# Optimization experiments

Measured on AMD Instinct MI355X. Metric: run time of the kernel, lower is better.

The kernel has to match this reference:

```python
import jax, jax.numpy as jnp
import numpy as np

BETA = 0.5
THR = 1.0
BN_EPS = 1e-5

@jax.custom_vjp
def spike(x):
    # heaviside fire: spk = 1[x > 0]
    return (x > 0).astype(x.dtype)

def _spike_fwd(x):
    return spike(x), x

def _spike_bwd(x, g):
    # snnTorch surrogate.atan(), alpha=2: grad = (alpha/2) / (1 + (pi/2*alpha*x)^2) = 1/(1+(pi*x)^2)
    return (g / (1.0 + (jnp.pi * x) ** 2),)

spike.defvjp(_spike_fwd, _spike_bwd)

def setup_inputs() -> dict:
    key = jax.random.key(0)
    ks = jax.random.split(key, 6)
    B, T, D, O = 512, 128, 512, 10
    data = jax.random.normal(ks[0], (B, T, D), dtype=jnp.float32)
    # deterministic Dropout(0.5) mask in {0, 2} (scaled by 1/keep_prob), time-major
    u = jax.random.uniform(ks[1], (T, B, D), dtype=jnp.float32)
    drop_mask = (u > 0.5).astype(jnp.float32) * 2.0
    W1 = jax.random.normal(ks[2], (D, D), dtype=jnp.float32) / np.sqrt(D)
    b1 = jax.random.normal(ks[3], (D,), dtype=jnp.float32) * 0.01
    gamma = jnp.ones((D,), dtype=jnp.float32)
    bn_beta = jnp.zeros((D,), dtype=jnp.float32)
    W2 = jax.random.normal(ks[4], (O, D), dtype=jnp.float32) / np.sqrt(D)
    b2 = jax.random.normal(ks[5], (O,), dtype=jnp.float32) * 0.01
    return {"data": data, "drop_mask": drop_mask, "W1": W1, "b1": b1,
            "gamma": gamma, "bn_beta": bn_beta, "W2": W2, "b2": b2}

def reference(data, drop_mask, W1, b1, gamma, bn_beta, W2, b2):
    B, T, D = data.shape
    O = W2.shape[0]
    xs = jnp.transpose(data, (1, 0, 2))  # [T, B, D] time-major

    def batchnorm(x):  # training-mode BatchNorm1d over batch dim
        mean = jnp.mean(x, axis=0)
        var = jnp.mean((x - mean) ** 2, axis=0)
        return gamma * (x - mean) * jax.lax.rsqrt(var + BN_EPS) + bn_beta

    def step(carry, inp):
        mem1, spk1, mem2, spk2 = carry
        xt, mt = inp
        cur1 = batchnorm((mt * xt) @ W1.T + b1)          # dropout -> linear -> BN
        mem1 = BETA * mem1 + cur1 - spk1 * THR           # Leaky, subtract reset
        spk1 = spike(mem1 - THR)
        cur2 = spk1 @ W2.T + b2
        mem2 = BETA * mem2 + cur2 - spk2 * THR
        spk2 = spike(mem2 - THR)
        return (mem1, spk1, mem2, spk2), spk2

    init = (jnp.zeros((B, D), data.dtype), jnp.zeros((B, D), data.dtype),
            jnp.zeros((B, O), data.dtype), jnp.zeros((B, O), data.dtype))
    _, spk_rec = jax.lax.scan(step, init, (xs, drop_mask))
    return spk_rec  # [T, B, out_size] == torch.stack(spk_rec)
```

## Files before the change

kernel.cpp:

```cpp
#include <hip/hip_runtime.h>
#include <math.h>

#define B_ 512
#define T_ 128
#define D_ 512
#define O_ 10

typedef unsigned int uint32;
typedef unsigned long long uint64;
typedef short bf16x8 __attribute__((ext_vector_type(8)));
typedef float f32x4 __attribute__((ext_vector_type(4)));

__device__ __forceinline__ uint32 bf16rne(float f) {
    uint32 u = __float_as_uint(f);
    return (u + 0x7FFFu + ((u >> 16) & 1u)) >> 16;
}
__device__ __forceinline__ float bf16f(uint32 h) { return __uint_as_float(h << 16); }

__device__ __forceinline__ uint32 pkbf16(float lo, float hi) {
    return bf16rne(lo) | (bf16rne(hi) << 16);
}

__device__ __forceinline__ void gload16_lds(const void* g, void* l) {
    __builtin_amdgcn_global_load_lds(
        (const __attribute__((address_space(1))) unsigned int*)g,
        (__attribute__((address_space(3))) unsigned int*)l, 16, 0, 0);
}

__global__ __launch_bounds__(256)
void presplitW_kernel(const float* __restrict__ W1, unsigned short* __restrict__ Wsp)
{
    const int idx = blockIdx.x * 256 + threadIdx.x;
    const float4 v = *(const float4*)(W1 + (size_t)idx * 4);
    float vv[4] = {v.x, v.y, v.z, v.w};
    uint32 c0[4], c1[4], c2[4];
#pragma unroll
    for (int i = 0; i < 4; ++i) {
        c0[i] = bf16rne(vv[i]);
        float r = vv[i] - bf16f(c0[i]);
        c1[i] = bf16rne(r);
        float r2 = r - bf16f(c1[i]);
        c2[i] = bf16rne(r2);
    }
    const size_t base = (size_t)idx * 4;
    uint2 w;
    w.x = c0[0] | (c0[1] << 16); w.y = c0[2] | (c0[3] << 16);
    *(uint2*)(Wsp + base) = w;
    w.x = c1[0] | (c1[1] << 16); w.y = c1[2] | (c1[3] << 16);
    *(uint2*)(Wsp + 262144 + base) = w;
    w.x = c2[0] | (c2[1] << 16); w.y = c2[2] | (c2[3] << 16);
    *(uint2*)(Wsp + 524288 + base) = w;
}

#define SPW 32
#define SPL (128*SPW)

__global__ __launch_bounds__(256)
void gemm1_kernel(const float* __restrict__ data, const float* __restrict__ drop,
                  const unsigned short* __restrict__ Wsp, const float* __restrict__ b1,
                  float* __restrict__ hbuf, double* __restrict__ pSum,
                  double* __restrict__ pSq, int t0, int Tc)
{
    __shared__ __align__(16) unsigned short As3[3 * SPL];
    __shared__ __align__(16) unsigned short Ws3[2][3 * SPL];

    const int tid = threadIdx.x;
    const int bid = blockIdx.x;
    const int xcd = bid & 7;
    const int rest = bid >> 3;
    const int yy = rest & 3;
    const int g = (rest >> 2) * 8 + xcd;

    const int R = g * 128;
    const int tc = R >> 9;
    const int b_base = R & 511;
    const int t = t0 + tc;
    const int d0 = yy * 128;

    const int w = tid >> 6;
    const int lane = tid & 63;
    const int wm = w & 1, wn = w >> 1;
    const int q = lane >> 4, r16 = lane & 15;

    f32x4 acc[4][4];
#pragma unroll
    for (int i = 0; i < 4; ++i)
#pragma unroll
        for (int j = 0; j < 4; ++j) acc[i][j] = (f32x4){0.f, 0.f, 0.f, 0.f};

    int dstA[2];
    const float* dsrc[2];
    const float* msrc[2];
#pragma unroll
    for (int i = 0; i < 2; ++i) {
        const int p = tid + i * 256;
        const int m = p >> 2;
        const int qg = p & 3;
        dstA[i] = m * SPW + (qg ^ ((m >> 1) & 3)) * 8;
        dsrc[i] = data + ((size_t)(b_base + m) * T_ + t) * D_ + qg * 8;
        msrc[i] = drop + ((size_t)t * B_ + b_base + m) * D_ + qg * 8;
    }

#define STAGE_W(K0, BUF)                                                        \
    {                                                                           \
        _Pragma("unroll")                                                       \
        for (int i_ = 0; i_ < 6; ++i_) {                                        \
            const int p_ = tid + i_ * 256;                                      \
            const int s_ = p_ >> 9;                                             \
            const int rem_ = p_ & 511;                                          \
            const int n_ = rem_ >> 2;                                           \
            const int qs_ = rem_ & 3;                                           \
            const int qg_ = qs_ ^ ((n_ >> 1) & 3);                              \
            gload16_lds(Wsp + (size_t)s_ * 262144 + (size_t)(d0 + n_) * 512     \
                            + (K0) + qg_ * 8,                                   \
                        &Ws3[BUF][(size_t)p_ * 8]);                             \
        }                                                                       \
    }

    STAGE_W(0, 0);
    float4 dR[2][2], mR[2][2];
#pragma unroll
    for (int i = 0; i < 2; ++i) {
        dR[i][0] = *(const float4*)(dsrc[i]);
        dR[i][1] = *(const float4*)(dsrc[i] + 4);
        mR[i][0] = *(const float4*)(msrc[i]);
        mR[i][1] = *(const float4*)(msrc[i] + 4);
    }

    int cur = 0;
    for (int ks = 0; ks < 16; ++ks) {
        const int k0 = ks * 32;
        if (ks < 15) STAGE_W(k0 + 32, cur ^ 1);

#pragma unroll
        for (int i = 0; i < 2; ++i) {
            float vv[8] = {dR[i][0].x*mR[i][0].x, dR[i][0].y*mR[i][0].y,
                           dR[i][0].z*mR[i][0].z, dR[i][0].w*mR[i][0].w,
                           dR[i][1].x*mR[i][1].x, dR[i][1].y*mR[i][1].y,
                           dR[i][1].z*mR[i][1].z, dR[i][1].w*mR[i][1].w};
            uint32 q0[4], q1[4], q2[4];
#pragma unroll
            for (int pr = 0; pr < 4; ++pr) {
                const float a = vv[2*pr], b = vv[2*pr+1];
                q0[pr] = pkbf16(a, b);
                const float ra = a - __uint_as_float(q0[pr] << 16);
                const float rb = b - __uint_as_float(q0[pr] & 0xFFFF0000u);
                q1[pr] = pkbf16(ra, rb);
                const float sa = ra - __uint_as_float(q1[pr] << 16);
                const float sb = rb - __uint_as_float(q1[pr] & 0xFFFF0000u);
                q2[pr] = pkbf16(sa, sb);
            }
            uint4 pk;
            pk.x = q0[0]; pk.y = q0[1]; pk.z = q0[2]; pk.w = q0[3];
            *(uint4*)(&As3[dstA[i]]) = pk;
            pk.x = q1[0]; pk.y = q1[1]; pk.z = q1[2]; pk.w = q1[3];
            *(uint4*)(&As3[SPL + dstA[i]]) = pk;
            pk.x = q2[0]; pk.y = q2[1]; pk.z = q2[2]; pk.w = q2[3];
            *(uint4*)(&As3[2*SPL + dstA[i]]) = pk;
        }

        if (ks < 15) {
            const int kn = k0 + 32;
#pragma unroll
            for (int i = 0; i < 2; ++i) {
                dR[i][0] = *(const float4*)(dsrc[i] + kn);
                dR[i][1] = *(const float4*)(dsrc[i] + kn + 4);
                mR[i][0] = *(const float4*)(msrc[i] + kn);
                mR[i][1] = *(const float4*)(msrc[i] + kn + 4);
            }
        }

        __builtin_amdgcn_sched_barrier(0);
        asm volatile("s_waitcnt lgkmcnt(0)");
        __builtin_amdgcn_s_barrier();
        __builtin_amdgcn_sched_barrier(0);

        const int qa = q ^ ((r16 >> 1) & 3);
        bf16x8 af[4][3], bfr[4][3];
#pragma unroll
        for (int mt = 0; mt < 4; ++mt)
#pragma unroll
            for (int s = 0; s < 3; ++s)
                af[mt][s] = *(const bf16x8*)(&As3[s*SPL + (wm*64 + mt*16 + r16)*SPW + qa*8]);
#pragma unroll
        for (int nt = 0; nt < 4; ++nt)
#pragma unroll
            for (int s = 0; s < 3; ++s)
                bfr[nt][s] = *(const bf16x8*)(&Ws3[cur][s*SPL + (wn*64 + nt*16 + r16)*SPW + qa*8]);

        __builtin_amdgcn_s_setprio(1);
#define PRODUCT(SA, SB)                                                          \
        {                                                                        \
            _Pragma("unroll")                                                    \
            for (int mt = 0; mt < 4; ++mt) {                                     \
                _Pragma("unroll")                                                \
                for (int nt = 0; nt < 4; ++nt)                                   \
                    acc[mt][nt] = __builtin_amdgcn_mfma_f32_16x16x32_bf16(       \
                        af[mt][SA], bfr[nt][SB], acc[mt][nt], 0, 0, 0);          \
            }                                                                    \
        }
        PRODUCT(0, 0)
        PRODUCT(0, 1)
        PRODUCT(1, 0)
        PRODUCT(1, 1)
        PRODUCT(0, 2)
        PRODUCT(2, 0)
#undef PRODUCT
        __builtin_amdgcn_s_setprio(0);

        __builtin_amdgcn_sched_barrier(0);
        __builtin_amdgcn_s_barrier();
        __builtin_amdgcn_sched_barrier(0);
        cur ^= 1;
    }
#undef STAGE_W

    float b1c[4];
#pragma unroll
    for (int nt = 0; nt < 4; ++nt) b1c[nt] = b1[d0 + wn*64 + nt*16 + r16];

    double sd[4], sq[4];
#pragma unroll
    for (int nt = 0; nt < 4; ++nt) { sd[nt] = 0.0; sq[nt] = 0.0; }

#pragma unroll
    for (int mt = 0; mt < 4; ++mt)
#pragma unroll
        for (int r = 0; r < 4; ++r) {
            const int row = R + wm*64 + mt*16 + q*4 + r;
            float* op = hbuf + (size_t)row * D_ + d0 + wn*64 + r16;
#pragma unroll
            for (int nt = 0; nt < 4; ++nt) {
                const float hf = acc[mt][nt][r] + b1c[nt];
                op[nt*16] = hf;
                const double dh = (double)hf;
                sd[nt] += dh;
                sq[nt] = fma(dh, dh, sq[nt]);
            }
        }
#pragma unroll
    for (int nt = 0; nt < 4; ++nt) {
        sd[nt] += __shfl_xor(sd[nt], 16); sd[nt] += __shfl_xor(sd[nt], 32);
        sq[nt] += __shfl_xor(sq[nt], 16); sq[nt] += __shfl_xor(sq[nt], 32);
    }
    double* dsh = (double*)&As3[0];
    __syncthreads();
    if (q == 0) {
#pragma unroll
        for (int nt = 0; nt < 4; ++nt) {
            dsh[(w*64 + nt*16 + r16)*2 + 0] = sd[nt];
            dsh[(w*64 + nt*16 + r16)*2 + 1] = sq[nt];
        }
    }
    __syncthreads();
    if (tid < 128) {
        const int col = tid;
        const int gg = col >> 6, c = col & 63;
        const double S = dsh[((2*gg)*64 + c)*2 + 0] + dsh[((2*gg+1)*64 + c)*2 + 0];
        const double Q = dsh[((2*gg)*64 + c)*2 + 1] + dsh[((2*gg+1)*64 + c)*2 + 1];
        const int bt = b_base >> 7;
        pSum[((size_t)(bt*Tc + tc))*D_ + d0 + col] = S;
        pSq [((size_t)(bt*Tc + tc))*D_ + d0 + col] = Q;
    }
}

__global__ __launch_bounds__(256)
void finalize_kernel(const double* __restrict__ pSum, const double* __restrict__ pSq,
                     const float* __restrict__ gamma, const float* __restrict__ bn_beta,
                     float* __restrict__ scaleArr, float* __restrict__ shiftArr, int Tc)
{
    const int tc = blockIdx.x;
    const int d = blockIdx.y * 256 + threadIdx.x;
    double S = 0.0, Q = 0.0;
#pragma unroll
    for (int bt = 0; bt < 4; ++bt) {
        S += pSum[((size_t)(bt * Tc + tc)) * D_ + d];
        Q += pSq [((size_t)(bt * Tc + tc)) * D_ + d];
    }
    const double mean = S / (double)B_;
    const double var  = Q / (double)B_ - mean * mean;
    const double rs   = 1.0 / sqrt(var + 1e-5);
    const double gm   = (double)gamma[d] * rs;
    scaleArr[tc * D_ + d] = (float)gm;
    shiftArr[tc * D_ + d] = (float)((double)bn_beta[d] - gm * mean);
}

__global__ __launch_bounds__(256)
void scanA_kernel(const float* __restrict__ hbuf, const float* __restrict__ scaleArr,
                  const float* __restrict__ shiftArr, uint64* __restrict__ spkM,
                  float* __restrict__ sMem1, float* __restrict__ sSpk1, int t0, int Tc)
{
    const int e = blockIdx.x * 256 + threadIdx.x;
    const int d = e & 511;
    const int lane = threadIdx.x & 63;
    const int mword = (e >> 6);

    float m1, s1;
    if (t0 == 0) { m1 = 0.f; s1 = 0.f; }
    else { m1 = sMem1[e]; s1 = sSpk1[e]; }

    float hv[4], sc[4], sf[4];
#pragma unroll
    for (int j = 0; j < 4; ++j) {
        const int tcj = (j < Tc) ? j : (Tc - 1);
        hv[j] = hbuf[(size_t)tcj * (B_ * D_) + e];
        sc[j] = scaleArr[tcj * D_ + d];
        sf[j] = shiftArr[tcj * D_ + d];
    }

    for (int tc = 0; tc < Tc; tc += 4) {
        float hvN[4], scN[4], sfN[4];
#pragma unroll
        for (int j = 0; j < 4; ++j) {
            int tn = tc + 4 + j; tn = (tn < Tc) ? tn : (Tc - 1);
            hvN[j] = hbuf[(size_t)tn * (B_ * D_) + e];
            scN[j] = scaleArr[tn * D_ + d];
            sfN[j] = shiftArr[tn * D_ + d];
        }
#pragma unroll
        for (int j = 0; j < 4; ++j) {
            if (tc + j < Tc) {
                const float cur1 = fmaf(sc[j], hv[j], sf[j]);
                m1 = fmaf(0.5f, m1, cur1) - s1;
                s1 = ((m1 - 1.0f) > 0.f) ? 1.f : 0.f;
                const uint64 mask = __ballot(s1 == 1.f);
                if (lane == 0)
                    spkM[(size_t)(tc + j) * (B_ * 8) + mword] = mask;
            }
        }
#pragma unroll
        for (int j = 0; j < 4; ++j) { hv[j] = hvN[j]; sc[j] = scN[j]; sf[j] = sfN[j]; }
    }

    sMem1[e] = m1;
    sSpk1[e] = s1;
}

__global__ __launch_bounds__(256)
void gemm2_kernel(const uint64* __restrict__ spkM, const float* __restrict__ W2,
                  const float* __restrict__ b2, float* __restrict__ cur2)
{
    const int g = blockIdx.x * 256 + threadIdx.x;
    const int row = g >> 3;
    const int i = g & 7;
    const unsigned char* sp = (const unsigned char*)spkM;

    float P[8][O_];
#pragma unroll
    for (int c = 0; c < 8; ++c) {
        const uint32 byte = sp[(size_t)row * 64 + c * 8 + i];
        float f[8];
#pragma unroll
        for (int j = 0; j < 8; ++j)
            f[j] = (byte & (1u << j)) ? 1.0f : 0.0f;
#pragma unroll
        for (int o = 0; o < O_; ++o) {
            const float* wp = W2 + o * D_ + (i + 8 * c) * 8;
            const float4 wa = *(const float4*)(wp);
            const float4 wb = *(const float4*)(wp + 4);
            float v = f[0] * wa.x;
            v = fmaf(f[1], wa.y, v); v = fmaf(f[2], wa.z, v); v = fmaf(f[3], wa.w, v);
            v = fmaf(f[4], wb.x, v); v = fmaf(f[5], wb.y, v); v = fmaf(f[6], wb.z, v);
            v = fmaf(f[7], wb.w, v);
            P[c][o] = v;
        }
    }

    float p[O_];
#pragma unroll
    for (int o = 0; o < O_; ++o) {
        const float a1 = P[0][o] + P[4][o];
        const float a2 = P[2][o] + P[6][o];
        const float a3 = P[1][o] + P[5][o];
        const float a4 = P[3][o] + P[7][o];
        p[o] = (a1 + a2) + (a3 + a4);
    }
#pragma unroll
    for (int o = 0; o < O_; ++o) {
        p[o] += __shfl_xor(p[o], 4);
        p[o] += __shfl_xor(p[o], 2);
        p[o] += __shfl_xor(p[o], 1);
    }

    float out0 = 0.f, out1 = 0.f;
#pragma unroll
    for (int o = 0; o < 8; ++o)
        if (i == o) out0 = p[o] + b2[o];
    if (i == 0) out1 = p[8] + b2[8];
    if (i == 1) out1 = p[9] + b2[9];
    cur2[(size_t)row * O_ + i] = out0;
    if (i < 2)
        cur2[(size_t)row * O_ + 8 + i] = out1;
}

__global__ __launch_bounds__(256)
void scanB_kernel(const float* __restrict__ cur2, float* __restrict__ out,
                  float* __restrict__ sMem2, float* __restrict__ sSpk2, int t0, int Tc)
{
    const int idx = blockIdx.x * 256 + threadIdx.x;
    float mem2, spk2;
    if (t0 == 0) { mem2 = 0.f; spk2 = 0.f; }
    else { mem2 = sMem2[idx]; spk2 = sSpk2[idx]; }

    float v[4], vn[4];
#pragma unroll
    for (int j = 0; j < 4; ++j) v[j] = cur2[(size_t)j * (B_ * O_) + idx];

    for (int tg = 0; tg < Tc; tg += 4) {
        if (tg + 4 < Tc) {
#pragma unroll
            for (int j = 0; j < 4; ++j)
                vn[j] = cur2[(size_t)(tg + 4 + j) * (B_ * O_) + idx];
        }
#pragma unroll
        for (int j = 0; j < 4; ++j) {
            mem2 = fmaf(0.5f, mem2, v[j]) - spk2;
            spk2 = ((mem2 - 1.0f) > 0.f) ? 1.f : 0.f;
            out[(size_t)(t0 + tg + j) * (B_ * O_) + idx] = spk2;
        }
#pragma unroll
        for (int j = 0; j < 4; ++j) v[j] = vn[j];
    }
    sMem2[idx] = mem2;
    sSpk2[idx] = spk2;
}

extern "C" void kernel_launch(void* const* d_in, const int* in_sizes, int n_in,
                              void* d_out, int out_size, void* d_ws, size_t ws_size,
                              hipStream_t stream) {
    const float* data    = (const float*)d_in[0];
    const float* drop    = (const float*)d_in[1];
    const float* W1      = (const float*)d_in[2];
    const float* b1      = (const float*)d_in[3];
    const float* gamma   = (const float*)d_in[4];
    const float* bn_beta = (const float*)d_in[5];
    const float* W2      = (const float*)d_in[6];
    const float* b2      = (const float*)d_in[7];
    float* out = (float*)d_out;

    const size_t fixedBytes = 1572864 + 2*1048576 + 2*20480;
    const size_t perT = 1048576 + 32768 + 20480 + 4096 + 32768;
    int Tc = T_;
    while (Tc > 2 && fixedBytes + (size_t)Tc * perT > ws_size) Tc >>= 1;

    char* p = (char*)d_ws;
    double* pSum    = (double*)p; p += (size_t)4 * Tc * D_ * 8;
    double* pSq     = (double*)p; p += (size_t)4 * Tc * D_ * 8;
    float* hbuf     = (float*)p; p += (size_t)Tc * B_ * D_ * 4;
    float* scaleArr = (float*)p; p += (size_t)Tc * D_ * 4;
    float* shiftArr = (float*)p; p += (size_t)Tc * D_ * 4;
    float* sMem1    = (float*)p; p += (size_t)B_ * D_ * 4;
    float* sSpk1    = (float*)p; p += (size_t)B_ * D_ * 4;
    float* sMem2    = (float*)p; p += (size_t)B_ * O_ * 4;
    float* sSpk2    = (float*)p; p += (size_t)B_ * O_ * 4;
    float* cur2     = (float*)p; p += (size_t)Tc * B_ * O_ * 4;
    unsigned short* Wsp = (unsigned short*)p; p += (size_t)3 * D_ * D_ * 2;
    uint64* spkM    = (uint64*)p; p += (size_t)Tc * B_ * 8 * 8;

    presplitW_kernel<<<256, 256, 0, stream>>>(W1, Wsp);

    for (int t0 = 0; t0 < T_; t0 += Tc) {
        gemm1_kernel<<<Tc * 16, 256, 0, stream>>>(data, drop, Wsp, b1, hbuf,
                                                  pSum, pSq, t0, Tc);
        finalize_kernel<<<dim3(Tc, D_ / 256), 256, 0, stream>>>(
            pSum, pSq, gamma, bn_beta, scaleArr, shiftArr, Tc);
        scanA_kernel<<<(B_ * D_) / 256, 256, 0, stream>>>(hbuf, scaleArr, shiftArr, spkM,
                                                          sMem1, sSpk1, t0, Tc);
        gemm2_kernel<<<Tc * 16, 256, 0, stream>>>(spkM, W2, b2, cur2);
        scanB_kernel<<<20, 256, 0, stream>>>(cur2, out, sMem2, sSpk2, t0, Tc);
    }
}
```

Before: 506.6 us.

## Fuse BN finalize into scan and gemm2 with output scan, use atomic stats

The per-batch-tile partial sums for the batch-norm statistics are now accumulated with double-precision atomics into a single per-time buffer. The separate finalize kernel is removed, and scanA recomputes the BN scale and shift inline in double precision for every element. gemm2 and scanB are merged into one kernel per batch row that keeps cur2 in LDS, removing the cur2 global buffer and two launches. In exchange, scanA does redundant double-precision divides and sqrt per element, the fused scan runs serially on only 10 threads per block, and double atomics add contention.

```diff
diff --git a/kernel.cpp b/kernel.cpp
--- a/kernel.cpp
+++ b/kernel.cpp
@@ -28,9 +28,11 @@
 }
 
 __global__ __launch_bounds__(256)
-void presplitW_kernel(const float* __restrict__ W1, unsigned short* __restrict__ Wsp)
+void presplitW_kernel(const float* __restrict__ W1, unsigned short* __restrict__ Wsp,
+                      double* __restrict__ pSum, double* __restrict__ pSq, int nAcc)
 {
     const int idx = blockIdx.x * 256 + threadIdx.x;
+    if (idx < nAcc) { pSum[idx] = 0.0; pSq[idx] = 0.0; }
     const float4 v = *(const float4*)(W1 + (size_t)idx * 4);
     float vv[4] = {v.x, v.y, v.z, v.w};
     uint32 c0[4], c1[4], c2[4];
@@ -258,36 +260,15 @@
         const int gg = col >> 6, c = col & 63;
         const double S = dsh[((2*gg)*64 + c)*2 + 0] + dsh[((2*gg+1)*64 + c)*2 + 0];
         const double Q = dsh[((2*gg)*64 + c)*2 + 1] + dsh[((2*gg+1)*64 + c)*2 + 1];
-        const int bt = b_base >> 7;
-        pSum[((size_t)(bt*Tc + tc))*D_ + d0 + col] = S;
-        pSq [((size_t)(bt*Tc + tc))*D_ + d0 + col] = Q;
+        atomicAdd(&pSum[tc * D_ + d0 + col], S);
+        atomicAdd(&pSq [tc * D_ + d0 + col], Q);
     }
 }
 
 __global__ __launch_bounds__(256)
-void finalize_kernel(const double* __restrict__ pSum, const double* __restrict__ pSq,
-                     const float* __restrict__ gamma, const float* __restrict__ bn_beta,
-                     float* __restrict__ scaleArr, float* __restrict__ shiftArr, int Tc)
-{
-    const int tc = blockIdx.x;
-    const int d = blockIdx.y * 256 + threadIdx.x;
-    double S = 0.0, Q = 0.0;
-#pragma unroll
-    for (int bt = 0; bt < 4; ++bt) {
-        S += pSum[((size_t)(bt * Tc + tc)) * D_ + d];
-        Q += pSq [((size_t)(bt * Tc + tc)) * D_ + d];
-    }
-    const double mean = S / (double)B_;
-    const double var  = Q / (double)B_ - mean * mean;
-    const double rs   = 1.0 / sqrt(var + 1e-5);
-    const double gm   = (double)gamma[d] * rs;
-    scaleArr[tc * D_ + d] = (float)gm;
-    shiftArr[tc * D_ + d] = (float)((double)bn_beta[d] - gm * mean);
-}
-
-__global__ __launch_bounds__(256)
-void scanA_kernel(const float* __restrict__ hbuf, const float* __restrict__ scaleArr,
-                  const float* __restrict__ shiftArr, uint64* __restrict__ spkM,
+void scanA_kernel(const float* __restrict__ hbuf, const double* __restrict__ pSum,
+                  const double* __restrict__ pSq, const float* __restrict__ gamma,
+                  const float* __restrict__ bn_beta, uint64* __restrict__ spkM,
                   float* __restrict__ sMem1, float* __restrict__ sSpk1, int t0, int Tc)
 {
     const int e = blockIdx.x * 256 + threadIdx.x;
@@ -295,32 +276,41 @@
     const int lane = threadIdx.x & 63;
     const int mword = (e >> 6);
 
+    const double gmA = (double)gamma[d];
+    const double btA = (double)bn_beta[d];
+
     float m1, s1;
     if (t0 == 0) { m1 = 0.f; s1 = 0.f; }
     else { m1 = sMem1[e]; s1 = sSpk1[e]; }
 
-    float hv[4], sc[4], sf[4];
+    float hv[4]; double Sv[4], Qv[4];
 #pragma unroll
     for (int j = 0; j < 4; ++j) {
         const int tcj = (j < Tc) ? j : (Tc - 1);
         hv[j] = hbuf[(size_t)tcj * (B_ * D_) + e];
-        sc[j] = scaleArr[tcj * D_ + d];
-        sf[j] = shiftArr[tcj * D_ + d];
+        Sv[j] = pSum[tcj * D_ + d];
+        Qv[j] = pSq [tcj * D_ + d];
     }
 
     for (int tc = 0; tc < Tc; tc += 4) {
-        float hvN[4], scN[4], sfN[4];
+        float hvN[4]; double SvN[4], QvN[4];
 #pragma unroll
         for (int j = 0; j < 4; ++j) {
             int tn = tc + 4 + j; tn = (tn < Tc) ? tn : (Tc - 1);
             hvN[j] = hbuf[(size_t)tn * (B_ * D_) + e];
-            scN[j] = scaleArr[tn * D_ + d];
-            sfN[j] = shiftArr[tn * D_ + d];
+            SvN[j] = pSum[tn * D_ + d];
+            QvN[j] = pSq [tn * D_ + d];
         }
 #pragma unroll
         for (int j = 0; j < 4; ++j) {
             if (tc + j < Tc) {
-                const float cur1 = fmaf(sc[j], hv[j], sf[j]);
+                const double mean = Sv[j] / (double)B_;
+                const double var  = Qv[j] / (double)B_ - mean * mean;
+                const double rs   = 1.0 / sqrt(var + 1e-5);
+                const double gm   = gmA * rs;
+                const float sc = (float)gm;
+                const float sf = (float)(btA - gm * mean);
+                const float cur1 = fmaf(sc, hv[j], sf);
                 m1 = fmaf(0.5f, m1, cur1) - s1;
                 s1 = ((m1 - 1.0f) > 0.f) ? 1.f : 0.f;
                 const uint64 mask = __ballot(s1 == 1.f);
@@ -329,7 +319,7 @@
             }
         }
 #pragma unroll
-        for (int j = 0; j < 4; ++j) { hv[j] = hvN[j]; sc[j] = scN[j]; sf[j] = sfN[j]; }
+        for (int j = 0; j < 4; ++j) { hv[j] = hvN[j]; Sv[j] = SvN[j]; Qv[j] = QvN[j]; }
     }
 
     sMem1[e] = m1;
@@ -337,92 +327,68 @@
 }
 
 __global__ __launch_bounds__(256)
-void gemm2_kernel(const uint64* __restrict__ spkM, const float* __restrict__ W2,
-                  const float* __restrict__ b2, float* __restrict__ cur2)
+void gemm2scanB_kernel(const uint64* __restrict__ spkM, const float* __restrict__ W2,
+                       const float* __restrict__ b2, float* __restrict__ out,
+                       float* __restrict__ sMem2, float* __restrict__ sSpk2,
+                       double* __restrict__ pSum, double* __restrict__ pSq,
+                       int t0, int Tc)
 {
-    const int g = blockIdx.x * 256 + threadIdx.x;
-    const int row = g >> 3;
-    const int i = g & 7;
-    const unsigned char* sp = (const unsigned char*)spkM;
-
-    float P[8][O_];
-#pragma unroll
-    for (int c = 0; c < 8; ++c) {
-        const uint32 byte = sp[(size_t)row * 64 + c * 8 + i];
-        float f[8];
-#pragma unroll
-        for (int j = 0; j < 8; ++j)
-            f[j] = (byte & (1u << j)) ? 1.0f : 0.0f;
-#pragma unroll
-        for (int o = 0; o < O_; ++o) {
-            const float* wp = W2 + o * D_ + (i + 8 * c) * 8;
-            const float4 wa = *(const float4*)(wp);
-            const float4 wb = *(const float4*)(wp + 4);
-            float v = f[0] * wa.x;
-            v = fmaf(f[1], wa.y, v); v = fmaf(f[2], wa.z, v); v = fmaf(f[3], wa.w, v);
-            v = fmaf(f[4], wb.x, v); v = fmaf(f[5], wb.y, v); v = fmaf(f[6], wb.z, v);
-            v = fmaf(f[7], wb.w, v);
-            P[c][o] = v;
-        }
-    }
-
-    float p[O_];
-#pragma unroll
-    for (int o = 0; o < O_; ++o) {
-        const float a1 = P[0][o] + P[4][o];
-        const float a2 = P[2][o] + P[6][o];
-        const float a3 = P[1][o] + P[5][o];
-        const float a4 = P[3][o] + P[7][o];
-        p[o] = (a1 + a2) + (a3 + a4);
-    }
-#pragma unroll
-    for (int o = 0; o < O_; ++o) {
-        p[o] += __shfl_xor(p[o], 4);
-        p[o] += __shfl_xor(p[o], 2);
-        p[o] += __shfl_xor(p[o], 1);
-    }
-
-    float out0 = 0.f, out1 = 0.f;
-#pragma unroll
-    for (int o = 0; o < 8; ++o)
-        if (i == o) out0 = p[o] + b2[o];
-    if (i == 0) out1 = p[8] + b2[8];
-    if (i == 1) out1 = p[9] + b2[9];
-    cur2[(size_t)row * O_ + i] = out0;
-    if (i < 2)
-        cur2[(size_t)row * O_ + 8 + i] = out1;
-}
-
-__global__ __launch_bounds__(256)
-void scanB_kernel(const float* __restrict__ cur2, float* __restrict__ out,
-                  float* __restrict__ sMem2, float* __restrict__ sSpk2, int t0, int Tc)
-{
-    const int idx = blockIdx.x * 256 + threadIdx.x;
-    float mem2, spk2;
-    if (t0 == 0) { mem2 = 0.f; spk2 = 0.f; }
-    else { mem2 = sMem2[idx]; spk2 = sSpk2[idx]; }
-
-    float v[4], vn[4];
-#pragma unroll
-    for (int j = 0; j < 4; ++j) v[j] = cur2[(size_t)j * (B_ * O_) + idx];
-
-    for (int tg = 0; tg < Tc; tg += 4) {
-        if (tg + 4 < Tc) {
-#pragma unroll
-            for (int j = 0; j < 4; ++j)
-                vn[j] = cur2[(size_t)(tg + 4 + j) * (B_ * O_) + idx];
-        }
-#pragma unroll
-        for (int j = 0; j < 4; ++j) {
-            mem2 = fmaf(0.5f, mem2, v[j]) - spk2;
+    __shared__ float c2s[128][O_];
+    const int b = blockIdx.x;
+    const int tid = threadIdx.x;
+    const int t = tid >> 1;
+    const int oh = (tid & 1) * 5;
+
+    if (t < Tc) {
+        const int row = t * B_ + b;
+        uint64 mk[8];
+#pragma unroll
+        for (int c = 0; c < 8; ++c) mk[c] = spkM[(size_t)row * 8 + c];
+#pragma unroll
+        for (int oo = 0; oo < 5; ++oo) {
+            const int o = oh + oo;
+            float T[8];
+#pragma unroll
+            for (int i = 0; i < 8; ++i) {
+                float P[8];
+#pragma unroll
+                for (int c = 0; c < 8; ++c) {
+                    const uint32 byte = (uint32)(mk[c] >> (i * 8)) & 0xFFu;
+                    float f[8];
+#pragma unroll
+                    for (int j = 0; j < 8; ++j)
+                        f[j] = (byte & (1u << j)) ? 1.0f : 0.0f;
+                    const float* wp = W2 + o * D_ + (i + 8 * c) * 8;
+                    const float4 wa = *(const float4*)(wp);
+                    const float4 wb = *(const float4*)(wp + 4);
+                    float v = f[0] * wa.x;
+                    v = fmaf(f[1], wa.y, v); v = fmaf(f[2], wa.z, v); v = fmaf(f[3], wa.w, v);
+                    v = fmaf(f[4], wb.x, v); v = fmaf(f[5], wb.y, v); v = fmaf(f[6], wb.z, v);
+                    v = fmaf(f[7], wb.w, v);
+                    P[c] = v;
+                }
+                T[i] = ((P[0] + P[4]) + (P[2] + P[6])) + ((P[1] + P[5]) + (P[3] + P[7]));
+            }
+            const float p = ((T[0] + T[4]) + (T[2] + T[6])) + ((T[1] + T[5]) + (T[3] + T[7]));
+            c2s[t][o] = p + b2[o];
+        }
+    }
+    __syncthreads();
+    if (tid < O_) {
+        const int o = tid;
+        float mem2, spk2;
+        if (t0 == 0) { mem2 = 0.f; spk2 = 0.f; }
+        else { mem2 = sMem2[b * O_ + o]; spk2 = sSpk2[b * O_ + o]; }
+        for (int tt = 0; tt < Tc; ++tt) {
+            mem2 = fmaf(0.5f, mem2, c2s[tt][o]) - spk2;
             spk2 = ((mem2 - 1.0f) > 0.f) ? 1.f : 0.f;
-            out[(size_t)(t0 + tg + j) * (B_ * O_) + idx] = spk2;
-        }
-#pragma unroll
-        for (int j = 0; j < 4; ++j) v[j] = vn[j];
-    }
-    sMem2[idx] = mem2;
-    sSpk2[idx] = spk2;
+            out[(size_t)(t0 + tt) * (B_ * O_) + b * O_ + o] = spk2;
+        }
+        sMem2[b * O_ + o] = mem2;
+        sSpk2[b * O_ + o] = spk2;
+    }
+    const int idx = b * 256 + tid;
+    if (idx < Tc * D_) { pSum[idx] = 0.0; pSq[idx] = 0.0; }
 }
 
 extern "C" void kernel_launch(void* const* d_in, const int* in_sizes, int n_in,
@@ -439,34 +405,30 @@
     float* out = (float*)d_out;
 
     const size_t fixedBytes = 1572864 + 2*1048576 + 2*20480;
-    const size_t perT = 1048576 + 32768 + 20480 + 4096 + 32768;
+    const size_t perT = 1048576 + 32768 + 8192;
     int Tc = T_;
     while (Tc > 2 && fixedBytes + (size_t)Tc * perT > ws_size) Tc >>= 1;
 
     char* p = (char*)d_ws;
-    double* pSum    = (double*)p; p += (size_t)4 * Tc * D_ * 8;
-    double* pSq     = (double*)p; p += (size_t)4 * Tc * D_ * 8;
+    double* pSum    = (double*)p; p += (size_t)Tc * D_ * 8;
+    double* pSq     = (double*)p; p += (size_t)Tc * D_ * 8;
     float* hbuf     = (float*)p; p += (size_t)Tc * B_ * D_ * 4;
-    float* scaleArr = (float*)p; p += (size_t)Tc * D_ * 4;
-    float* shiftArr = (float*)p; p += (size_t)Tc * D_ * 4;
     float* sMem1    = (float*)p; p += (size_t)B_ * D_ * 4;
     float* sSpk1    = (float*)p; p += (size_t)B_ * D_ * 4;
     float* sMem2    = (float*)p; p += (size_t)B_ * O_ * 4;
     float* sSpk2    = (float*)p; p += (size_t)B_ * O_ * 4;
-    float* cur2     = (float*)p; p += (size_t)Tc * B_ * O_ * 4;
     unsigned short* Wsp = (unsigned short*)p; p += (size_t)3 * D_ * D_ * 2;
     uint64* spkM    = (uint64*)p; p += (size_t)Tc * B_ * 8 * 8;
 
-    presplitW_kernel<<<256, 256, 0, stream>>>(W1, Wsp);
+    presplitW_kernel<<<256, 256, 0, stream>>>(W1, Wsp, pSum, pSq, Tc * D_);
 
     for (int t0 = 0; t0 < T_; t0 += Tc) {
         gemm1_kernel<<<Tc * 16, 256, 0, stream>>>(data, drop, Wsp, b1, hbuf,
                                                   pSum, pSq, t0, Tc);
-        finalize_kernel<<<dim3(Tc, D_ / 256), 256, 0, stream>>>(
-            pSum, pSq, gamma, bn_beta, scaleArr, shiftArr, Tc);
-        scanA_kernel<<<(B_ * D_) / 256, 256, 0, stream>>>(hbuf, scaleArr, shiftArr, spkM,
-                                                          sMem1, sSpk1, t0, Tc);
-        gemm2_kernel<<<Tc * 16, 256, 0, stream>>>(spkM, W2, b2, cur2);
-        scanB_kernel<<<20, 256, 0, stream>>>(cur2, out, sMem2, sSpk2, t0, Tc);
-    }
-}
+        scanA_kernel<<<(B_ * D_) / 256, 256, 0, stream>>>(hbuf, pSum, pSq, gamma,
+                                                          bn_beta, spkM, sMem1, sSpk1,
+                                                          t0, Tc);
+        gemm2scanB_kernel<<<B_, 256, 0, stream>>>(spkM, W2, b2, out, sMem2, sSpk2,
+                                                  pSum, pSq, t0, Tc);
+    }
+}
```

Result: slower. 572.6 us (+13.0%).

## Build GEMM A fragments directly in registers instead of staging through LDS

Applied to the files above, without the earlier changes.

The masked input tile is now loaded by each wave straight from global memory in MFMA fragment order. It is split into three bf16 parts in registers rather than written to a shared As3 buffer and read back. This removes the As3 LDS buffer, its writes and reads, and the barrier that sat between producing and consuming A. The W barrier's reuse of that buffer's space for the reduction scratch moves to Ws3. In exchange, the two waves that share the same rows both load and convert those rows, which doubles global A traffic and the split arithmetic per block. Removing that barrier also risks a race on the asynchronously loaded W buffer if no other synchronisation remains in the loop.

```diff
diff --git a/kernel.cpp b/kernel.cpp
--- a/kernel.cpp
+++ b/kernel.cpp
@@ -61,7 +61,6 @@
                   float* __restrict__ hbuf, double* __restrict__ pSum,
                   double* __restrict__ pSq, int t0, int Tc)
 {
-    __shared__ __align__(16) unsigned short As3[3 * SPL];
     __shared__ __align__(16) unsigned short Ws3[2][3 * SPL];
 
     const int tid = threadIdx.x;
@@ -88,18 +87,11 @@
 #pragma unroll
         for (int j = 0; j < 4; ++j) acc[i][j] = (f32x4){0.f, 0.f, 0.f, 0.f};
 
-    int dstA[2];
-    const float* dsrc[2];
-    const float* msrc[2];
-#pragma unroll
-    for (int i = 0; i < 2; ++i) {
-        const int p = tid + i * 256;
-        const int m = p >> 2;
-        const int qg = p & 3;
-        dstA[i] = m * SPW + (qg ^ ((m >> 1) & 3)) * 8;
-        dsrc[i] = data + ((size_t)(b_base + m) * T_ + t) * D_ + qg * 8;
-        msrc[i] = drop + ((size_t)t * B_ + b_base + m) * D_ + qg * 8;
-    }
+    const int row0 = b_base + wm * 64 + r16;
+    const float* dsrc0 = data + ((size_t)row0 * T_ + t) * D_ + q * 8;
+    const float* msrc0 = drop + ((size_t)t * B_ + row0) * D_ + q * 8;
+    const size_t dStride = (size_t)16 * T_ * D_;
+    const size_t mStride = (size_t)16 * D_;
 
 #define STAGE_W(K0, BUF)                                                        \
     {                                                                           \
@@ -118,13 +110,13 @@
     }
 
     STAGE_W(0, 0);
-    float4 dR[2][2], mR[2][2];
-#pragma unroll
-    for (int i = 0; i < 2; ++i) {
-        dR[i][0] = *(const float4*)(dsrc[i]);
-        dR[i][1] = *(const float4*)(dsrc[i] + 4);
-        mR[i][0] = *(const float4*)(msrc[i]);
-        mR[i][1] = *(const float4*)(msrc[i] + 4);
+    float4 dR[4][2], mR[4][2];
+#pragma unroll
+    for (int mt = 0; mt < 4; ++mt) {
+        dR[mt][0] = *(const float4*)(dsrc0 + (size_t)mt * dStride);
+        dR[mt][1] = *(const float4*)(dsrc0 + (size_t)mt * dStride + 4);
+        mR[mt][0] = *(const float4*)(msrc0 + (size_t)mt * mStride);
+        mR[mt][1] = *(const float4*)(msrc0 + (size_t)mt * mStride + 4);
     }
 
     int cur = 0;
@@ -132,12 +124,13 @@
         const int k0 = ks * 32;
         if (ks < 15) STAGE_W(k0 + 32, cur ^ 1);
 
-#pragma unroll
-        for (int i = 0; i < 2; ++i) {
-            float vv[8] = {dR[i][0].x*mR[i][0].x, dR[i][0].y*mR[i][0].y,
-                           dR[i][0].z*mR[i][0].z, dR[i][0].w*mR[i][0].w,
-                           dR[i][1].x*mR[i][1].x, dR[i][1].y*mR[i][1].y,
-                           dR[i][1].z*mR[i][1].z, dR[i][1].w*mR[i][1].w};
+        bf16x8 af[4][3];
+#pragma unroll
+        for (int mt = 0; mt < 4; ++mt) {
+            float vv[8] = {dR[mt][0].x*mR[mt][0].x, dR[mt][0].y*mR[mt][0].y,
+                           dR[mt][0].z*mR[mt][0].z, dR[mt][0].w*mR[mt][0].w,
+                           dR[mt][1].x*mR[mt][1].x, dR[mt][1].y*mR[mt][1].y,
+                           dR[mt][1].z*mR[mt][1].z, dR[mt][1].w*mR[mt][1].w};
             uint32 q0[4], q1[4], q2[4];
 #pragma unroll
             for (int pr = 0; pr < 4; ++pr) {
@@ -150,43 +143,32 @@
                 const float sb = rb - __uint_as_float(q1[pr] & 0xFFFF0000u);
                 q2[pr] = pkbf16(sa, sb);
             }
-            uint4 pk;
-            pk.x = q0[0]; pk.y = q0[1]; pk.z = q0[2]; pk.w = q0[3];
-            *(uint4*)(&As3[dstA[i]]) = pk;
-            pk.x = q1[0]; pk.y = q1[1]; pk.z = q1[2]; pk.w = q1[3];
-            *(uint4*)(&As3[SPL + dstA[i]]) = pk;
-            pk.x = q2[0]; pk.y = q2[1]; pk.z = q2[2]; pk.w = q2[3];
-            *(uint4*)(&As3[2*SPL + dstA[i]]) = pk;
-        }
+            union { uint32 u[4]; bf16x8 v; } c0, c1, c2;
+#pragma unroll
+            for (int pr = 0; pr < 4; ++pr) {
+                c0.u[pr] = q0[pr]; c1.u[pr] = q1[pr]; c2.u[pr] = q2[pr];
+            }
+            af[mt][0] = c0.v; af[mt][1] = c1.v; af[mt][2] = c2.v;
+        }
+
+        const int qa = q ^ ((r16 >> 1) & 3);
+        bf16x8 bfr[4][3];
+#pragma unroll
+        for (int nt = 0; nt < 4; ++nt)
+#pragma unroll
+            for (int s = 0; s < 3; ++s)
+                bfr[nt][s] = *(const bf16x8*)(&Ws3[cur][s*SPL + (wn*64 + nt*16 + r16)*SPW + qa*8]);
 
         if (ks < 15) {
             const int kn = k0 + 32;
 #pragma unroll
-            for (int i = 0; i < 2; ++i) {
-                dR[i][0] = *(const float4*)(dsrc[i] + kn);
-                dR[i][1] = *(const float4*)(dsrc[i] + kn + 4);
-                mR[i][0] = *(const float4*)(msrc[i] + kn);
-                mR[i][1] = *(const float4*)(msrc[i] + kn + 4);
+            for (int mt = 0; mt < 4; ++mt) {
+                dR[mt][0] = *(const float4*)(dsrc0 + (size_t)mt * dStride + kn);
+                dR[mt][1] = *(const float4*)(dsrc0 + (size_t)mt * dStride + kn + 4);
+                mR[mt][0] = *(const float4*)(msrc0 + (size_t)mt * mStride + kn);
+                mR[mt][1] = *(const float4*)(msrc0 + (size_t)mt * mStride + kn + 4);
             }
         }
-
-        __builtin_amdgcn_sched_barrier(0);
-        asm volatile("s_waitcnt lgkmcnt(0)");
-        __builtin_amdgcn_s_barrier();
-        __builtin_amdgcn_sched_barrier(0);
-
-        const int qa = q ^ ((r16 >> 1) & 3);
-        bf16x8 af[4][3], bfr[4][3];
-#pragma unroll
-        for (int mt = 0; mt < 4; ++mt)
-#pragma unroll
-            for (int s = 0; s < 3; ++s)
-                af[mt][s] = *(const bf16x8*)(&As3[s*SPL + (wm*64 + mt*16 + r16)*SPW + qa*8]);
-#pragma unroll
-        for (int nt = 0; nt < 4; ++nt)
-#pragma unroll
-            for (int s = 0; s < 3; ++s)
-                bfr[nt][s] = *(const bf16x8*)(&Ws3[cur][s*SPL + (wn*64 + nt*16 + r16)*SPW + qa*8]);
 
         __builtin_amdgcn_s_setprio(1);
 #define PRODUCT(SA, SB)                                                          \
@@ -243,7 +225,7 @@
         sd[nt] += __shfl_xor(sd[nt], 16); sd[nt] += __shfl_xor(sd[nt], 32);
         sq[nt] += __shfl_xor(sq[nt], 16); sq[nt] += __shfl_xor(sq[nt], 32);
     }
-    double* dsh = (double*)&As3[0];
+    double* dsh = (double*)&Ws3[0][0];
     __syncthreads();
     if (q == 0) {
 #pragma unroll
```

Result: slower. 684.8 us (+35.2%).
